# Kernel tuning notes

Measured on AMD Instinct MI355X. Metric: run time of the kernel, lower is better.

## Reference

```python
import jax, jax.numpy as jnp
import numpy as np
from jax import lax

B, C_IN, T = 256, 1, 1632
HID, CB_DIM, NUM_TOK, NUM_Q = 64, 512, 1024, 2


def conv_k2s2(x, W, b):
    # Conv1d(kernel=2, stride=2): x [B,Ci,T] -> [B,Co,T//2]; W [Co,Ci,2]
    Bx, Ci, Tx = x.shape
    xr = x.reshape(Bx, Ci, Tx // 2, 2)
    return jnp.einsum('bitk,oik->bot', xr, W) + b[None, :, None]


def convT_k2s2(x, W, b):
    # ConvTranspose1d(kernel=2, stride=2): x [B,Ci,T] -> [B,Co,2T]; W [Ci,Co,2] (torch layout)
    Bx, Ci, Tx = x.shape
    y = jnp.einsum('bit,iok->botk', x, W)  # [B,Co,T,2]
    Co = W.shape[1]
    return y.reshape(Bx, Co, 2 * Tx) + b[None, :, None]


def conv1x1(x, W, b):
    # W [Co,Ci]
    return jnp.einsum('bit,oi->bot', x, W) + b[None, :, None]


def residual_vq(x, codebooks):
    # x [B,t,D]; codebooks [NUM_Q, NUM_TOK, D]. Euclidean argmin + straight-through.
    residual = x
    quantized_out = jnp.zeros_like(x)
    all_idx, all_loss = [], []
    for q in range(codebooks.shape[0]):
        cb = codebooks[q]  # [N,D]
        # squared euclidean distance, single large GEMM
        d2 = (jnp.sum(residual ** 2, -1, keepdims=True)
              - 2.0 * jnp.einsum('btd,nd->btn', residual, cb)
              + jnp.sum(cb ** 2, -1))  # [B,t,N]
        idx = jnp.argmin(d2, axis=-1)  # [B,t]
        quant = cb[idx]  # gather [B,t,D]
        # commitment loss (codebook treated as fixed / EMA-updated)
        loss = jnp.mean((lax.stop_gradient(quant) - residual) ** 2)
        # straight-through estimator
        quant_st = residual + lax.stop_gradient(quant - residual)
        residual = residual - lax.stop_gradient(quant)
        quantized_out = quantized_out + quant_st
        all_idx.append(idx)
        all_loss.append(loss)
    return quantized_out, jnp.stack(all_idx, -1), jnp.stack(all_loss)


def setup_inputs() -> dict:
    key = jax.random.key(0)
    ks = jax.random.split(key, 16)
    s = 0.02
    return {
        'img': jax.random.normal(ks[0], (B, C_IN, T), jnp.float32),
        'W_e1': jax.random.normal(ks[1], (HID, C_IN, 2), jnp.float32) * s,
        'b_e1': jnp.zeros((HID,), jnp.float32),
        'W_e2': jax.random.normal(ks[2], (HID, HID, 2), jnp.float32) * s,
        'b_e2': jnp.zeros((HID,), jnp.float32),
        'W_e3': jax.random.normal(ks[3], (CB_DIM, HID), jnp.float32) * s,
        'b_e3': jnp.zeros((CB_DIM,), jnp.float32),
        'codebooks': jax.random.normal(ks[4], (NUM_Q, NUM_TOK, CB_DIM), jnp.float32),
        'Wt_d1': jax.random.normal(ks[5], (CB_DIM, HID, 2), jnp.float32) * s,
        'b_d1': jnp.zeros((HID,), jnp.float32),
        'Wt_d2': jax.random.normal(ks[6], (HID, HID, 2), jnp.float32) * s,
        'b_d2': jnp.zeros((HID,), jnp.float32),
        'W_d3': jax.random.normal(ks[7], (C_IN, HID), jnp.float32) * s,
        'b_d3': jnp.zeros((C_IN,), jnp.float32),
    }


def reference(img, W_e1, b_e1, W_e2, b_e2, W_e3, b_e3, codebooks,
              Wt_d1, b_d1, Wt_d2, b_d2, W_d3, b_d3):
    # encoder
    h = jax.nn.relu(conv_k2s2(img, W_e1, b_e1))
    h = jax.nn.relu(conv_k2s2(h, W_e2, b_e2))
    encoded = conv1x1(h, W_e3, b_e3)  # [B,512,408]
    # residual VQ over tokens
    x = jnp.transpose(encoded, (0, 2, 1))  # b c t -> b t c
    quantized, indices, commit_loss = residual_vq(x, codebooks)
    quantized = jnp.transpose(quantized, (0, 2, 1))  # b t c -> b c t
    # decoder
    d = jax.nn.relu(convT_k2s2(quantized, Wt_d1, b_d1))
    d = jax.nn.relu(convT_k2s2(d, Wt_d2, b_d2))
    out = conv1x1(d, W_d3, b_d3)  # [B,1,1632]
    recon_loss = jnp.mean((img - out) ** 2)
    return out, recon_loss, commit_loss, indices, quantized
```

## Files before the change

### kernel.cpp

```cpp
#include <hip/hip_runtime.h>

#define NB    256
#define TLEN  1632
#define HIDC  64
#define CBD   512
#define NTOK  1024
#define T2L   816
#define T4L   408
#define MTOK  (NB*T4L)
#define M2TOK (NB*T2L)
#define MOUT  (NB*TLEN)

#define DO_OUT    ((size_t)0)
#define DO_RECON  ((size_t)417792)
#define DO_IDX    ((size_t)417795)
#define DO_QUANT  ((size_t)626691)

typedef unsigned short u16;
typedef unsigned long long u64;
typedef __attribute__((ext_vector_type(8))) short short8;
typedef __attribute__((ext_vector_type(4))) float f32x4;
typedef __attribute__((ext_vector_type(8))) _Float16 half8;
typedef __attribute__((ext_vector_type(4))) _Float16 half4;

static constexpr size_t OFF_XR  = 0;
static constexpr size_t OFF_H1  = OFF_XR + (size_t)MTOK*512;
static constexpr size_t OFF_H2  = OFF_H1 + (size_t)NB*T2L*64;
static constexpr size_t OFF_BE2 = OFF_H2 + (size_t)NB*T4L*64;
static constexpr size_t OFF_BD1 = OFF_BE2 + 8192;
static constexpr size_t OFF_BD2 = OFF_BD1 + 65536;
static constexpr size_t OFF_BX1 = OFF_BD2 + 8192;
static constexpr size_t OFF_BX2 = OFF_BX1 + 128;
static constexpr size_t OFF_ZB  = OFF_BX2 + 128;
static constexpr size_t OFF_C2  = OFF_ZB + 128;
static constexpr size_t OFF_SLOT= OFF_C2 + 2048;
static constexpr size_t OFF_IDXI= OFF_SLOT + 1536;
static constexpr size_t OFF_KEYS= OFF_IDXI + (size_t)MTOK*2;
static constexpr size_t OFF_FC  = OFF_KEYS + (size_t)MTOK*4;
static constexpr size_t OFF_FLAG= OFF_FC + 4;
static constexpr size_t OFF_CBH = OFF_FLAG + (size_t)MTOK*2;
static constexpr size_t OFF_CBL = OFF_CBH + 524288;
static constexpr size_t OFF_P0  = OFF_CBL + 524288;
static constexpr size_t OFF_P1  = OFF_P0 + 131072;
static constexpr size_t OFF_PAIRS = OFF_P1 + 131072;

__device__ inline u64 shfl_xor_u64_w16(u64 v, int m) {
    unsigned lo = (unsigned)v, hi = (unsigned)(v >> 32);
    lo = __shfl_xor(lo, m, 16);
    hi = __shfl_xor(hi, m, 16);
    return (((u64)hi) << 32) | lo;
}
__device__ inline u64 packkey(float d, int n) {
    unsigned u = __float_as_uint(d);
    u = (u & 0x80000000u) ? ~u : (u | 0x80000000u);
    return (((u64)u) << 32) | (unsigned)n;
}
__device__ inline float unpackd(u64 k) {
    unsigned u = (unsigned)(k >> 32);
    u = (u & 0x80000000u) ? (u & 0x7fffffffu) : ~u;
    return __uint_as_float(u);
}
__device__ inline void merge2(u64& k1, u64& k2, u64 o1, u64 o2) {
    u64 n1 = (k1 < o1) ? k1 : o1;
    u64 hi = (k1 < o1) ? o1 : k1;
    u64 cand = (k1 <= o1) ? k2 : o2;
    u64 n2 = (hi < cand) ? hi : cand;
    k1 = n1; k2 = n2;
}
__device__ inline half4 cvt_h4(float4 v) {
    half4 h;
    h.x = (_Float16)v.x; h.y = (_Float16)v.y;
    h.z = (_Float16)v.z; h.w = (_Float16)v.w;
    return h;
}
__device__ inline half8 cvt_h8(float4 v0, float4 v1) {
    half8 h;
    h[0] = (_Float16)v0.x; h[1] = (_Float16)v0.y;
    h[2] = (_Float16)v0.z; h[3] = (_Float16)v0.w;
    h[4] = (_Float16)v1.x; h[5] = (_Float16)v1.y;
    h[6] = (_Float16)v1.z; h[7] = (_Float16)v1.w;
    return h;
}
__device__ inline void gll16(const u16* g, u16* l) {
    __builtin_amdgcn_global_load_lds((const __attribute__((address_space(1))) void*)g,
                                     (__attribute__((address_space(3))) void*)l, 16, 0, 0);
}

__global__ void setup_kernel(const float* __restrict__ We2, const float* __restrict__ Wtd1,
                             const float* __restrict__ Wtd2, const float* __restrict__ bd1,
                             const float* __restrict__ bd2, const float* __restrict__ cbs,
                             float* __restrict__ Be2, float* __restrict__ Bd1,
                             float* __restrict__ Bd2, float* __restrict__ bx1, float* __restrict__ bx2,
                             u16* __restrict__ cbh, float* __restrict__ c2) {
    size_t t = (size_t)blockIdx.x * 256 + threadIdx.x;
    {
        float4 v = *(const float4*)(cbs + t * 4);
        *(half4*)&cbh[t * 4] = cvt_h4(v);
    }
    {
        int w = (int)(t >> 6);
        int lane = threadIdx.x & 63;
        if (w < 2048) {
            const float* r = cbs + (size_t)w * 512;
            float4 a = *(const float4*)(r + lane * 8);
            float4 b = *(const float4*)(r + lane * 8 + 4);
            float s = a.x*a.x + a.y*a.y + a.z*a.z + a.w*a.w + b.x*b.x + b.y*b.y + b.z*b.z + b.w*b.w;
            #pragma unroll
            for (int o = 32; o > 0; o >>= 1) s += __shfl_down(s, o, 64);
            if (lane == 0) c2[w] = s;
        }
    }
    size_t stride = (size_t)gridDim.x * 256;
    for (size_t x = t; x < 64 * 128; x += stride) {
        int c = (int)(x >> 7), k = (int)(x & 127);
        Be2[x] = We2[c * 128 + ((k & 63) << 1) + (k >> 6)];
    }
    for (size_t x = t; x < 128 * 512; x += stride) {
        int n = (int)(x >> 9), k = (int)(x & 511);
        Bd1[x] = Wtd1[k * 128 + n];
    }
    for (size_t x = t; x < 128 * 64; x += stride) {
        int n = (int)(x >> 6), k = (int)(x & 63);
        Bd2[x] = Wtd2[k * 128 + n];
    }
    for (size_t x = t; x < 128; x += stride) { bx1[x] = bd1[x >> 1]; bx2[x] = bd2[x >> 1]; }
}

__global__ void enc1_kernel(const float* __restrict__ img, const float* __restrict__ W,
                            const float* __restrict__ bias, float* __restrict__ h1) {
    int idx = blockIdx.x * 256 + threadIdx.x;
    int c = idx & 63;
    int t = (idx >> 6) % T2L;
    int b = idx / (64 * T2L);
    float v = W[c * 2] * img[(size_t)b * TLEN + 2 * t] +
              W[c * 2 + 1] * img[(size_t)b * TLEN + 2 * t + 1] + bias[c];
    h1[idx] = fmaxf(v, 0.f);
}

__global__ __launch_bounds__(256) void gemm_nt(const float* __restrict__ A, const float* __restrict__ Bw,
                        const float* __restrict__ bias, float* __restrict__ C,
                        int M, int N, int K, int amode, int relu) {
    __shared__ float As[32][132];
    __shared__ float Bs[32][68];
    int m0 = blockIdx.x * 128;
    int n0 = blockIdx.y * 64;
    int tid = threadIdx.x;
    int tx = tid & 15;
    int ty = tid >> 4;
    float acc[8][4];
    #pragma unroll
    for (int i = 0; i < 8; ++i)
        #pragma unroll
        for (int j = 0; j < 4; ++j) acc[i][j] = 0.f;

    for (int k0 = 0; k0 < K; k0 += 32) {
        #pragma unroll
        for (int i = 0; i < 4; ++i) {
            int idx = tid + i * 256;
            int row = idx >> 3;
            int kq = idx & 7;
            int m = m0 + row;
            size_t base;
            if (amode == 0) base = (size_t)m * K;
            else            base = (size_t)(((m / T4L) * T2L + 2 * (m % T4L)) * 64);
            float4 v = *(const float4*)(A + base + k0 + kq * 4);
            int kk = kq * 4;
            As[kk + 0][row] = v.x; As[kk + 1][row] = v.y;
            As[kk + 2][row] = v.z; As[kk + 3][row] = v.w;
        }
        #pragma unroll
        for (int i = 0; i < 2; ++i) {
            int idx = tid + i * 256;
            int row = idx >> 3;
            int kq = idx & 7;
            float4 v = *(const float4*)(Bw + (size_t)(n0 + row) * K + k0 + kq * 4);
            int kk = kq * 4;
            Bs[kk + 0][row] = v.x; Bs[kk + 1][row] = v.y;
            Bs[kk + 2][row] = v.z; Bs[kk + 3][row] = v.w;
        }
        __syncthreads();
        #pragma unroll
        for (int kk = 0; kk < 32; ++kk) {
            float a[8], bf[4];
            float4 a0 = *(const float4*)&As[kk][ty * 8];
            float4 a1 = *(const float4*)&As[kk][ty * 8 + 4];
            a[0]=a0.x; a[1]=a0.y; a[2]=a0.z; a[3]=a0.w;
            a[4]=a1.x; a[5]=a1.y; a[6]=a1.z; a[7]=a1.w;
            float4 b0 = *(const float4*)&Bs[kk][tx * 4];
            bf[0]=b0.x; bf[1]=b0.y; bf[2]=b0.z; bf[3]=b0.w;
            #pragma unroll
            for (int i = 0; i < 8; ++i)
                #pragma unroll
                for (int j = 0; j < 4; ++j) acc[i][j] += a[i] * bf[j];
        }
        __syncthreads();
    }
    #pragma unroll
    for (int i = 0; i < 8; ++i) {
        int m = m0 + ty * 8 + i;
        float4 v;
        v.x = acc[i][0] + bias[n0 + tx * 4 + 0];
        v.y = acc[i][1] + bias[n0 + tx * 4 + 1];
        v.z = acc[i][2] + bias[n0 + tx * 4 + 2];
        v.w = acc[i][3] + bias[n0 + tx * 4 + 3];
        if (relu) { v.x=fmaxf(v.x,0.f); v.y=fmaxf(v.y,0.f); v.z=fmaxf(v.z,0.f); v.w=fmaxf(v.w,0.f); }
        *(float4*)(C + (size_t)m * N + n0 + tx * 4) = v;
    }
}

template<int Q1>
__global__ __launch_bounds__(256, 2) void vq_f16_db(
    const float* __restrict__ Ap, const u16* __restrict__ cbh,
    const float* __restrict__ c2, const u64* __restrict__ prevkeys,
    const u16* __restrict__ cb0h, u64* __restrict__ pairs)
{
    __shared__ __align__(16) u16 As[2][128 * 40];
    __shared__ __align__(16) u16 Bs[2][256 * 32];
    int tid = threadIdx.x;
    int n0 = blockIdx.x * 256, m0 = blockIdx.y * 128;
    int lane = tid & 63, wid = tid >> 6;
    int lm = lane & 15, quad = lane >> 4;
    int wm = wid >> 1, wn = wid & 1;

    f32x4 acc[4][8];
    #pragma unroll
    for (int i = 0; i < 4; ++i)
        #pragma unroll
        for (int j = 0; j < 8; ++j) acc[i][j] = (f32x4){0.f, 0.f, 0.f, 0.f};

    int ar[2], acq[2], coffA[2];
    #pragma unroll
    for (int i = 0; i < 2; ++i) {
        int idx = tid + i * 256;
        ar[i] = idx >> 2; acq[i] = idx & 3;
        coffA[i] = 0;
        if (Q1) coffA[i] = (int)(prevkeys[m0 + ar[i]] & 0xFFFFFFFFull) * 512;
    }
    int brow[4], bchk[4];
    #pragma unroll
    for (int i = 0; i < 4; ++i) {
        brow[i] = i * 64 + wid * 16 + (lane >> 2);
        bchk[i] = (lane & 3) ^ ((brow[i] >> 1) & 3);
    }

#define VQ_GLLB(BUF, K0)                                                              \
    _Pragma("unroll")                                                                 \
    for (int i = 0; i < 4; ++i) {                                                     \
        const u16* gp = cbh + (size_t)(n0 + brow[i]) * 512 + (K0) + bchk[i] * 8;      \
        gll16(gp, &Bs[BUF][i * 2048 + wid * 512]);                                    \
    }

#define VQ_LOADA(K0, V0, V1, CH)                                                      \
    _Pragma("unroll")                                                                 \
    for (int i = 0; i < 2; ++i) {                                                     \
        const float* s = Ap + (size_t)(m0 + ar[i]) * 512 + (K0) + acq[i] * 8;         \
        V0[i] = *(const float4*)s;                                                    \
        V1[i] = *(const float4*)(s + 4);                                              \
        if (Q1) CH[i] = *(const half8*)(cb0h + coffA[i] + (K0) + acq[i] * 8);         \
    }

#define VQ_WRITEA(BUF, V0, V1, CH)                                                    \
    _Pragma("unroll")                                                                 \
    for (int i = 0; i < 2; ++i) {                                                     \
        half8 hv = cvt_h8(V0[i], V1[i]);                                              \
        if (Q1) hv = hv - CH[i];                                                      \
        *(half8*)&As[BUF][ar[i] * 40 + acq[i] * 8] = hv;                              \
    }

#define VQ_COMPUTE(BUF) {                                                             \
        half8 ah[4];                                                                  \
        _Pragma("unroll")                                                             \
        for (int mt = 0; mt < 4; ++mt)                                                \
            ah[mt] = *(const half8*)&As[BUF][(wm*64 + mt*16 + lm) * 40 + quad * 8];   \
        _Pragma("unroll")                                                             \
        for (int nt = 0; nt < 8; ++nt) {                                              \
            int rn = wn * 128 + nt * 16 + lm;                                         \
            half8 bh = *(const half8*)&Bs[BUF][rn * 32 + ((quad ^ ((rn >> 1) & 3)) * 8)]; \
            _Pragma("unroll")                                                         \
            for (int mt = 0; mt < 4; ++mt)                                            \
                acc[mt][nt] = __builtin_amdgcn_mfma_f32_16x16x32_f16(ah[mt], bh, acc[mt][nt], 0, 0, 0); \
        }                                                                             \
    }

    float4 v0A[2], v1A[2], v0B[2], v1B[2];
    half8 chA[2], chB[2];
    (void)chA; (void)chB;

    VQ_GLLB(0, 0);
    VQ_LOADA(0, v0A, v1A, chA);
    VQ_WRITEA(0, v0A, v1A, chA);
    VQ_LOADA(32, v0B, v1B, chB);
    __syncthreads();

    for (int tp = 0; tp < 8; ++tp) {
        {
            VQ_GLLB(1, (2 * tp + 1) * 32);
            VQ_WRITEA(1, v0B, v1B, chB);
            if (tp < 7) { VQ_LOADA((2 * tp + 2) * 32, v0A, v1A, chA); }
            VQ_COMPUTE(0);
            __syncthreads();
        }
        {
            if (tp < 7) {
                VQ_GLLB(0, (2 * tp + 2) * 32);
                VQ_WRITEA(0, v0A, v1A, chA);
                VQ_LOADA((2 * tp + 3) * 32, v0B, v1B, chB);
            }
            VQ_COMPUTE(1);
            __syncthreads();
        }
    }
#undef VQ_GLLB
#undef VQ_LOADA
#undef VQ_WRITEA
#undef VQ_COMPUTE

    float c2v[8];
    #pragma unroll
    for (int nt = 0; nt < 8; ++nt) c2v[nt] = c2[n0 + wn * 128 + nt * 16 + lm];

    u64* scr = (u64*)&As[0][0];
    #pragma unroll
    for (int mt = 0; mt < 4; ++mt) {
        #pragma unroll
        for (int rg = 0; rg < 4; ++rg) {
            int tl = wm * 64 + mt * 16 + quad * 4 + rg;
            u64 k1 = ~0ull, k2 = ~0ull;
            #pragma unroll
            for (int nt = 0; nt < 8; ++nt) {
                float d = c2v[nt] - 2.0f * acc[mt][nt][rg];
                u64 k = packkey(d, n0 + wn * 128 + nt * 16 + lm);
                if (k < k1) { k2 = k1; k1 = k; } else if (k < k2) { k2 = k; }
            }
            #pragma unroll
            for (int s = 1; s < 16; s <<= 1) {
                u64 o1 = shfl_xor_u64_w16(k1, s);
                u64 o2 = shfl_xor_u64_w16(k2, s);
                merge2(k1, k2, o1, o2);
            }
            if (lm == 0) { scr[wn * 256 + tl * 2] = k1; scr[wn * 256 + tl * 2 + 1] = k2; }
        }
    }
    __syncthreads();
    if (tid < 128) {
        u64 a1 = scr[tid * 2], a2 = scr[tid * 2 + 1];
        merge2(a1, a2, scr[256 + tid * 2], scr[256 + tid * 2 + 1]);
        size_t base = (size_t)(m0 + tid) * 8 + blockIdx.x * 2;
        pairs[base] = a1; pairs[base + 1] = a2;
    }
}

__global__ void vq_reduce(const u64* __restrict__ pairs, u64* __restrict__ keybuf,
                          int* __restrict__ fc, int* __restrict__ flaglist, float tau) {
    int m = blockIdx.x * 256 + threadIdx.x;
    const u64* p = pairs + (size_t)m * 8;
    u64 k1 = ~0ull, k2 = ~0ull;
    #pragma unroll
    for (int i = 0; i < 8; ++i) {
        u64 k = p[i];
        if (k < k1) { k2 = k1; k1 = k; } else if (k < k2) { k2 = k; }
    }
    keybuf[m] = k1;
    if (unpackd(k2) - unpackd(k1) < tau) {
        int pos = atomicAdd(fc, 1);
        flaglist[pos] = m;
    }
}

__global__ void vq_rescue(const float* __restrict__ xr, const float* __restrict__ cb,
                          const float* __restrict__ c2, const float* __restrict__ cb0,
                          const u64* __restrict__ prevkeys,
                          const int* __restrict__ fc, const int* __restrict__ flaglist,
                          u64* __restrict__ keybuf) {
    __shared__ u64 red[4];
    int cnt = *fc;
    int lane = threadIdx.x & 63, wid = threadIdx.x >> 6;
    for (int f = blockIdx.x; f < cnt; f += gridDim.x) {
        int m = flaglist[f];
        float4 rv0 = *(const float4*)(xr + (size_t)m * 512 + lane * 8);
        float4 rv1 = *(const float4*)(xr + (size_t)m * 512 + lane * 8 + 4);
        if (cb0) {
            size_t co = (size_t)(prevkeys[m] & 0xFFFFFFFFull) * 512;
            float4 c0 = *(const float4*)(cb0 + co + lane * 8);
            float4 c1 = *(const float4*)(cb0 + co + lane * 8 + 4);
            rv0.x -= c0.x; rv0.y -= c0.y; rv0.z -= c0.z; rv0.w -= c0.w;
            rv1.x -= c1.x; rv1.y -= c1.y; rv1.z -= c1.z; rv1.w -= c1.w;
        }
        u64 best = ~0ull;
        for (int c = wid * 256; c < wid * 256 + 256; ++c) {
            const float* cp = cb + (size_t)c * 512 + lane * 8;
            float4 c0 = *(const float4*)cp;
            float4 c1 = *(const float4*)(cp + 4);
            float p = rv0.x*c0.x + rv0.y*c0.y + rv0.z*c0.z + rv0.w*c0.w
                    + rv1.x*c1.x + rv1.y*c1.y + rv1.z*c1.z + rv1.w*c1.w;
            #pragma unroll
            for (int s = 1; s < 64; s <<= 1) p += __shfl_xor(p, s, 64);
            u64 k = packkey(c2[c] - 2.0f * p, c);
            if (k < best) best = k;
        }
        if (lane == 0) red[wid] = best;
        __syncthreads();
        if (threadIdx.x == 0) {
            u64 b = red[0];
            if (red[1] < b) b = red[1];
            if (red[2] < b) b = red[2];
            if (red[3] < b) b = red[3];
            keybuf[m] = b;
        }
        __syncthreads();
    }
}

__global__ void commit_idx_kernel(const float* __restrict__ xr,
                                  const float* __restrict__ cb0f, const float* __restrict__ cb1f,
                                  const u64* __restrict__ keys0, const u64* __restrict__ keys1,
                                  float* __restrict__ idx_f, int* __restrict__ idx_i,
                                  float* __restrict__ slots) {
    int tid = threadIdx.x;
    int lane = tid & 63;
    int m = blockIdx.x * 4 + (tid >> 6);
    unsigned i0 = (unsigned)(keys0[m] & 0xFFFFFFFFull);
    unsigned i1 = (unsigned)(keys1[m] & 0xFFFFFFFFull);
    const float* x = xr + (size_t)m * 512 + lane * 8;
    const float* c0 = cb0f + (size_t)i0 * 512 + lane * 8;
    const float* c1 = cb1f + (size_t)i1 * 512 + lane * 8;
    float4 x0 = *(const float4*)x, x1 = *(const float4*)(x + 4);
    float4 a0 = *(const float4*)c0, a1 = *(const float4*)(c0 + 4);
    float4 b0 = *(const float4*)c1, b1 = *(const float4*)(c1 + 4);
    x0.x -= a0.x; x0.y -= a0.y; x0.z -= a0.z; x0.w -= a0.w;
    x1.x -= a1.x; x1.y -= a1.y; x1.z -= a1.z; x1.w -= a1.w;
    float s1 = x0.x*x0.x + x0.y*x0.y + x0.z*x0.z + x0.w*x0.w
             + x1.x*x1.x + x1.y*x1.y + x1.z*x1.z + x1.w*x1.w;
    x0.x -= b0.x; x0.y -= b0.y; x0.z -= b0.z; x0.w -= b0.w;
    x1.x -= b1.x; x1.y -= b1.y; x1.z -= b1.z; x1.w -= b1.w;
    float s2 = x0.x*x0.x + x0.y*x0.y + x0.z*x0.z + x0.w*x0.w
             + x1.x*x1.x + x1.y*x1.y + x1.z*x1.z + x1.w*x1.w;
    #pragma unroll
    for (int o = 32; o > 0; o >>= 1) { s1 += __shfl_down(s1, o, 64); s2 += __shfl_down(s2, o, 64); }
    if (lane == 0) {
        atomicAdd(&slots[512 + (m & 511)], s1);
        atomicAdd(&slots[1024 + (m & 511)], s2);
        idx_f[(size_t)m * 2]     = (float)i0;
        idx_f[(size_t)m * 2 + 1] = (float)i1;
        idx_i[m * 2] = (int)i0;
        idx_i[m * 2 + 1] = (int)i1;
    }
}

__global__ void quant_out_kernel(const float* __restrict__ cb0, const float* __restrict__ cb1,
                                 const int* __restrict__ idxi, float* __restrict__ out4) {
    __shared__ float buf[64][129];
    __shared__ int i0s[64], i1s[64];
    int b = blockIdx.x;
    int t0 = blockIdx.y * 64;
    int c0 = blockIdx.z * 128;
    int tid = threadIdx.x;
    if (tid < 64) {
        int t = t0 + tid;
        int i0 = 0, i1 = 0;
        if (t < T4L) { i0 = idxi[(b * T4L + t) * 2]; i1 = idxi[(b * T4L + t) * 2 + 1]; }
        i0s[tid] = i0; i1s[tid] = i1;
    }
    __syncthreads();
    int cl = tid & 127, th = tid >> 7;
    for (int t = th; t < 64; t += 2) {
        if (t0 + t < T4L)
            buf[t][cl] = cb0[(size_t)i0s[t] * 512 + c0 + cl] + cb1[(size_t)i1s[t] * 512 + c0 + cl];
    }
    __syncthreads();
    int lane = tid & 63, ch = tid >> 6;
    for (int cc = ch; cc < 128; cc += 4) {
        int t = t0 + lane;
        if (t < T4L) out4[((size_t)b * 512 + c0 + cc) * T4L + t] = buf[lane][cc];
    }
}

__global__ void d1_gather_kernel(const float* __restrict__ P0, const float* __restrict__ P1,
                                 const int* __restrict__ idxi, const float* __restrict__ bx1,
                                 float* __restrict__ d1) {
    int x = blockIdx.x * 256 + threadIdx.x;
    int n = x & 127;
    int m = x >> 7;
    int b = m / T4L, t = m % T4L;
    int i0 = idxi[m * 2], i1 = idxi[m * 2 + 1];
    float v = P0[i0 * 128 + n] + P1[i1 * 128 + n] + bx1[n];
    v = fmaxf(v, 0.f);
    d1[((size_t)(b * T2L + 2 * t + (n & 1))) * 64 + (n >> 1)] = v;
}

__global__ __launch_bounds__(256) void dec2_fused(
    const float* __restrict__ d1, const float* __restrict__ Bd2, const float* __restrict__ bx2,
    const float* __restrict__ W3, const float* __restrict__ b3, const float* __restrict__ img,
    float* __restrict__ out, float* __restrict__ slots)
{
    __shared__ float As[32][132];
    __shared__ float Bs[32][132];
    __shared__ float w3s[64];
    int m0 = blockIdx.x * 128;
    int tid = threadIdx.x;
    int tx = tid & 15;
    int ty = tid >> 4;
    if (tid < 64) w3s[tid] = W3[tid];
    float acc[8][8];
    #pragma unroll
    for (int i = 0; i < 8; ++i)
        #pragma unroll
        for (int j = 0; j < 8; ++j) acc[i][j] = 0.f;

    for (int k0 = 0; k0 < 64; k0 += 32) {
        #pragma unroll
        for (int i = 0; i < 4; ++i) {
            int idx = tid + i * 256;
            int row = idx >> 3;
            int kq = idx & 7;
            float4 v = *(const float4*)(d1 + (size_t)(m0 + row) * 64 + k0 + kq * 4);
            int kk = kq * 4;
            As[kk + 0][row] = v.x; As[kk + 1][row] = v.y;
            As[kk + 2][row] = v.z; As[kk + 3][row] = v.w;
        }
        #pragma unroll
        for (int i = 0; i < 4; ++i) {
            int idx = tid + i * 256;
            int row = idx >> 3;
            int kq = idx & 7;
            float4 v = *(const float4*)(Bd2 + (size_t)row * 64 + k0 + kq * 4);
            int kk = kq * 4;
            Bs[kk + 0][row] = v.x; Bs[kk + 1][row] = v.y;
            Bs[kk + 2][row] = v.z; Bs[kk + 3][row] = v.w;
        }
        __syncthreads();
        #pragma unroll
        for (int kk = 0; kk < 32; ++kk) {
            float a[8], bf[8];
            float4 a0 = *(const float4*)&As[kk][ty * 8];
            float4 a1 = *(const float4*)&As[kk][ty * 8 + 4];
            a[0]=a0.x; a[1]=a0.y; a[2]=a0.z; a[3]=a0.w;
            a[4]=a1.x; a[5]=a1.y; a[6]=a1.z; a[7]=a1.w;
            float4 b0 = *(const float4*)&Bs[kk][tx * 4];
            float4 b1 = *(const float4*)&Bs[kk][64 + tx * 4];
            bf[0]=b0.x; bf[1]=b0.y; bf[2]=b0.z; bf[3]=b0.w;
            bf[4]=b1.x; bf[5]=b1.y; bf[6]=b1.z; bf[7]=b1.w;
            #pragma unroll
            for (int i = 0; i < 8; ++i)
                #pragma unroll
                for (int j = 0; j < 8; ++j) acc[i][j] += a[i] * bf[j];
        }
        __syncthreads();
    }
    float bb3 = b3[0];
    float local = 0.f;
    #pragma unroll
    for (int i = 0; i < 8; ++i) {
        float s0 = 0.f, s1 = 0.f;
        #pragma unroll
        for (int j = 0; j < 4; ++j) {
            int n = tx * 4 + j;
            float v = fmaxf(acc[i][j] + bx2[n], 0.f);
            float w = w3s[n >> 1];
            if (j & 1) s1 += w * v; else s0 += w * v;
            int n2 = 64 + tx * 4 + j;
            float v2 = fmaxf(acc[i][j + 4] + bx2[n2], 0.f);
            float w2 = w3s[n2 >> 1];
            if (j & 1) s1 += w2 * v2; else s0 += w2 * v2;
        }
        #pragma unroll
        for (int o = 8; o > 0; o >>= 1) { s0 += __shfl_down(s0, o, 16); s1 += __shfl_down(s1, o, 16); }
        if (tx == 0) {
            int m = m0 + ty * 8 + i;
            int b = m / T2L, t2 = m % T2L;
            size_t o0 = (size_t)b * TLEN + 2 * t2;
            float v0 = s0 + bb3, v1 = s1 + bb3;
            out[o0] = v0; out[o0 + 1] = v1;
            float e0 = img[o0] - v0, e1 = img[o0 + 1] - v1;
            local += e0 * e0 + e1 * e1;
        }
    }
    if (tx == 0) atomicAdd(&slots[(blockIdx.x * 16 + ty) & 511], local);
}

__global__ void finalize_kernel(const float* __restrict__ slots, float* __restrict__ out_scalars) {
    __shared__ float red[256];
    int tid = threadIdx.x;
    for (int which = 0; which < 3; ++which) {
        float s = slots[which * 512 + tid] + slots[which * 512 + tid + 256];
        red[tid] = s; __syncthreads();
        for (int st = 128; st > 0; st >>= 1) { if (tid < st) red[tid] += red[tid + st]; __syncthreads(); }
        if (tid == 0) {
            float denom = (which == 0) ? (float)MOUT : (float)((size_t)MTOK * 512);
            out_scalars[which] = red[0] / denom;
        }
        __syncthreads();
    }
}

extern "C" void kernel_launch(void* const* d_in, const int* in_sizes, int n_in,
                              void* d_out, int out_size, void* d_ws, size_t ws_size,
                              hipStream_t stream) {
    const float* img  = (const float*)d_in[0];
    const float* We1  = (const float*)d_in[1];
    const float* be1  = (const float*)d_in[2];
    const float* We2  = (const float*)d_in[3];
    const float* be2  = (const float*)d_in[4];
    const float* We3  = (const float*)d_in[5];
    const float* be3  = (const float*)d_in[6];
    const float* cbs  = (const float*)d_in[7];
    const float* Wtd1 = (const float*)d_in[8];
    const float* bd1  = (const float*)d_in[9];
    const float* Wtd2 = (const float*)d_in[10];
    const float* bd2  = (const float*)d_in[11];
    const float* Wd3  = (const float*)d_in[12];
    const float* bd3  = (const float*)d_in[13];

    float* w = (float*)d_ws;
    float* xr   = w + OFF_XR;
    float* h1   = w + OFF_H1;
    float* h2   = w + OFF_H2;
    float* Be2  = w + OFF_BE2;
    float* Bd1  = w + OFF_BD1;
    float* Bd2  = w + OFF_BD2;
    float* bx1  = w + OFF_BX1;
    float* bx2  = w + OFF_BX2;
    float* zerob= w + OFF_ZB;
    float* c2   = w + OFF_C2;
    float* slots= w + OFF_SLOT;
    int*   idxi = (int*)(w + OFF_IDXI);
    u64*   keys = (u64*)(w + OFF_KEYS);
    int*   fc   = (int*)(w + OFF_FC);
    int*   flag = (int*)(w + OFF_FLAG);
    u16*   cbh  = (u16*)(w + OFF_CBH);
    float* P0   = w + OFF_P0;
    float* P1   = w + OFF_P1;
    u64*   pairs= (u64*)(w + OFF_PAIRS);

    float* outp = (float*)d_out;
    float* out0   = outp + DO_OUT;
    float* oscal  = outp + DO_RECON;
    float* idxf   = outp + DO_IDX;
    float* qout   = outp + DO_QUANT;

    hipMemsetAsync(slots, 0, 1536 * sizeof(float), stream);
    hipMemsetAsync(fc, 0, 2 * sizeof(int), stream);
    hipMemsetAsync(zerob, 0, 128 * sizeof(float), stream);

    setup_kernel<<<1024, 256, 0, stream>>>(We2, Wtd1, Wtd2, bd1, bd2, cbs,
                                           Be2, Bd1, Bd2, bx1, bx2, cbh, c2);

    const float* cb1p = cbs + (size_t)NTOK * CBD;

    gemm_nt<<<dim3(8, 2), 256, 0, stream>>>(cbs,  Bd1, zerob, P0, 1024, 128, 512, 0, 0);
    gemm_nt<<<dim3(8, 2), 256, 0, stream>>>(cb1p, Bd1, zerob, P1, 1024, 128, 512, 0, 0);

    enc1_kernel<<<(NB * T2L * HIDC) / 256, 256, 0, stream>>>(img, We1, be1, h1);
    gemm_nt<<<dim3(MTOK / 128, 1), 256, 0, stream>>>(h1, Be2, be2, h2, MTOK, 64, 128, 1, 1);
    gemm_nt<<<dim3(MTOK / 128, 8), 256, 0, stream>>>(h2, We3, be3, xr, MTOK, 512, 64, 0, 0);

    vq_f16_db<0><<<dim3(4, MTOK / 128), 256, 0, stream>>>(xr, cbh, c2, nullptr, nullptr, pairs);
    vq_reduce<<<MTOK / 256, 256, 0, stream>>>(pairs, keys, fc + 0, flag, 0.05f);
    vq_rescue<<<1024, 256, 0, stream>>>(xr, cbs, c2, nullptr, nullptr, fc + 0, flag, keys);
    vq_f16_db<1><<<dim3(4, MTOK / 128), 256, 0, stream>>>(xr, cbh + (size_t)NTOK * 512,
                                                          c2 + NTOK, keys, cbh, pairs);
    vq_reduce<<<MTOK / 256, 256, 0, stream>>>(pairs, keys + MTOK, fc + 1, flag + MTOK, 0.15f);
    vq_rescue<<<1024, 256, 0, stream>>>(xr, cb1p, c2 + NTOK, cbs, keys, fc + 1, flag + MTOK, keys + MTOK);

    commit_idx_kernel<<<MTOK / 4, 256, 0, stream>>>(xr, cbs, cb1p, keys, keys + MTOK, idxf, idxi, slots);

    quant_out_kernel<<<dim3(NB, 7, 4), 256, 0, stream>>>(cbs, cb1p, idxi, qout);

    d1_gather_kernel<<<(MTOK * 128) / 256, 256, 0, stream>>>(P0, P1, idxi, bx1, h1);
    dec2_fused<<<M2TOK / 128, 256, 0, stream>>>(h1, Bd2, bx2, Wd3, bd3, img, out0, slots);

    finalize_kernel<<<1, 256, 0, stream>>>(slots, oscal);
}
```

Measured before the change: 1.163 ms.

## Feed VQ GEMM with precomputed fp16 activations via direct global-to-LDS loads

The encoder's final GEMM epilogue now also writes an fp16 copy of the encoded tokens. A small r1_prep kernel computes the fp16 first-stage residual up front. Both VQ passes then stream their A operand with global_load_lds into a swizzled 32-wide LDS tile, instead of loading fp32, converting and storing through registers, which simplifies the double-buffered loop. The fp16 scratch lives in the not-yet-written idx/quant region of the output buffer. The costs are an extra kernel, extra fp16 writes, and dependence on that region being overwritten later.

```diff
diff --git a/kernel.cpp b/kernel.cpp
--- a/kernel.cpp
+++ b/kernel.cpp
@@ -15,6 +15,8 @@
 #define DO_RECON  ((size_t)417792)
 #define DO_IDX    ((size_t)417795)
 #define DO_QUANT  ((size_t)626691)
+#define DO_XRH    ((size_t)417796)
+#define DO_R1H    (DO_XRH + (size_t)MTOK*256)
 
 typedef unsigned short u16;
 typedef unsigned long long u64;
@@ -73,14 +75,6 @@
     h.z = (_Float16)v.z; h.w = (_Float16)v.w;
     return h;
 }
-__device__ inline half8 cvt_h8(float4 v0, float4 v1) {
-    half8 h;
-    h[0] = (_Float16)v0.x; h[1] = (_Float16)v0.y;
-    h[2] = (_Float16)v0.z; h[3] = (_Float16)v0.w;
-    h[4] = (_Float16)v1.x; h[5] = (_Float16)v1.y;
-    h[6] = (_Float16)v1.z; h[7] = (_Float16)v1.w;
-    return h;
-}
 __device__ inline void gll16(const u16* g, u16* l) {
     __builtin_amdgcn_global_load_lds((const __attribute__((address_space(1))) void*)g,
                                      (__attribute__((address_space(3))) void*)l, 16, 0, 0);
@@ -139,7 +133,7 @@
 
 __global__ __launch_bounds__(256) void gemm_nt(const float* __restrict__ A, const float* __restrict__ Bw,
                         const float* __restrict__ bias, float* __restrict__ C,
-                        int M, int N, int K, int amode, int relu) {
+                        int M, int N, int K, int amode, int relu, u16* __restrict__ xh) {
     __shared__ float As[32][132];
     __shared__ float Bs[32][68];
     int m0 = blockIdx.x * 128;
@@ -205,16 +199,27 @@
         v.w = acc[i][3] + bias[n0 + tx * 4 + 3];
         if (relu) { v.x=fmaxf(v.x,0.f); v.y=fmaxf(v.y,0.f); v.z=fmaxf(v.z,0.f); v.w=fmaxf(v.w,0.f); }
         *(float4*)(C + (size_t)m * N + n0 + tx * 4) = v;
-    }
-}
-
-template<int Q1>
-__global__ __launch_bounds__(256, 2) void vq_f16_db(
-    const float* __restrict__ Ap, const u16* __restrict__ cbh,
-    const float* __restrict__ c2, const u64* __restrict__ prevkeys,
-    const u16* __restrict__ cb0h, u64* __restrict__ pairs)
+        if (xh) *(half4*)&xh[(size_t)m * N + n0 + tx * 4] = cvt_h4(v);
+    }
+}
+
+__global__ void r1_prep(const u16* __restrict__ xrh, const u16* __restrict__ cbh0,
+                        const u64* __restrict__ keys, u16* __restrict__ r1h) {
+    int m = blockIdx.x * 8 + (threadIdx.x >> 5);
+    int l = threadIdx.x & 31;
+    int i0 = (int)(keys[m] & 0xFFFFFFFFull);
+    const half8* xp = (const half8*)(xrh + (size_t)m * 512 + l * 16);
+    const half8* cp = (const half8*)(cbh0 + (size_t)i0 * 512 + l * 16);
+    half8* rp = (half8*)(r1h + (size_t)m * 512 + l * 16);
+    rp[0] = xp[0] - cp[0];
+    rp[1] = xp[1] - cp[1];
+}
+
+__global__ __launch_bounds__(256, 2) void vq_f16_gll(
+    const u16* __restrict__ Ah, const u16* __restrict__ cbh,
+    const float* __restrict__ c2, u64* __restrict__ pairs)
 {
-    __shared__ __align__(16) u16 As[2][128 * 40];
+    __shared__ __align__(16) u16 As[2][128 * 32];
     __shared__ __align__(16) u16 Bs[2][256 * 32];
     int tid = threadIdx.x;
     int n0 = blockIdx.x * 256, m0 = blockIdx.y * 128;
@@ -228,13 +233,12 @@
         #pragma unroll
         for (int j = 0; j < 8; ++j) acc[i][j] = (f32x4){0.f, 0.f, 0.f, 0.f};
 
-    int ar[2], acq[2], coffA[2];
+    int arow[2], achk[2];
     #pragma unroll
     for (int i = 0; i < 2; ++i) {
-        int idx = tid + i * 256;
-        ar[i] = idx >> 2; acq[i] = idx & 3;
-        coffA[i] = 0;
-        if (Q1) coffA[i] = (int)(prevkeys[m0 + ar[i]] & 0xFFFFFFFFull) * 512;
+        int slot = wid * 128 + i * 64 + lane;
+        arow[i] = slot >> 2;
+        achk[i] = (slot & 3) ^ ((arow[i] >> 1) & 3);
     }
     int brow[4], bchk[4];
     #pragma unroll
@@ -243,35 +247,25 @@
         bchk[i] = (lane & 3) ^ ((brow[i] >> 1) & 3);
     }
 
-#define VQ_GLLB(BUF, K0)                                                              \
-    _Pragma("unroll")                                                                 \
-    for (int i = 0; i < 4; ++i) {                                                     \
-        const u16* gp = cbh + (size_t)(n0 + brow[i]) * 512 + (K0) + bchk[i] * 8;      \
-        gll16(gp, &Bs[BUF][i * 2048 + wid * 512]);                                    \
-    }
-
-#define VQ_LOADA(K0, V0, V1, CH)                                                      \
-    _Pragma("unroll")                                                                 \
-    for (int i = 0; i < 2; ++i) {                                                     \
-        const float* s = Ap + (size_t)(m0 + ar[i]) * 512 + (K0) + acq[i] * 8;         \
-        V0[i] = *(const float4*)s;                                                    \
-        V1[i] = *(const float4*)(s + 4);                                              \
-        if (Q1) CH[i] = *(const half8*)(cb0h + coffA[i] + (K0) + acq[i] * 8);         \
-    }
-
-#define VQ_WRITEA(BUF, V0, V1, CH)                                                    \
-    _Pragma("unroll")                                                                 \
-    for (int i = 0; i < 2; ++i) {                                                     \
-        half8 hv = cvt_h8(V0[i], V1[i]);                                              \
-        if (Q1) hv = hv - CH[i];                                                      \
-        *(half8*)&As[BUF][ar[i] * 40 + acq[i] * 8] = hv;                              \
+#define VQ_GLL(BUF, K0)                                                               \
+    {                                                                                 \
+        _Pragma("unroll")                                                             \
+        for (int i = 0; i < 2; ++i)                                                   \
+            gll16(Ah + (size_t)(m0 + arow[i]) * 512 + (K0) + achk[i] * 8,             \
+                  &As[BUF][wid * 1024 + i * 512]);                                    \
+        _Pragma("unroll")                                                             \
+        for (int i = 0; i < 4; ++i)                                                   \
+            gll16(cbh + (size_t)(n0 + brow[i]) * 512 + (K0) + bchk[i] * 8,            \
+                  &Bs[BUF][i * 2048 + wid * 512]);                                    \
     }
 
 #define VQ_COMPUTE(BUF) {                                                             \
         half8 ah[4];                                                                  \
         _Pragma("unroll")                                                             \
-        for (int mt = 0; mt < 4; ++mt)                                                \
-            ah[mt] = *(const half8*)&As[BUF][(wm*64 + mt*16 + lm) * 40 + quad * 8];   \
+        for (int mt = 0; mt < 4; ++mt) {                                              \
+            int r = wm * 64 + mt * 16 + lm;                                           \
+            ah[mt] = *(const half8*)&As[BUF][r * 32 + ((quad ^ ((r >> 1) & 3)) * 8)]; \
+        }                                                                             \
         _Pragma("unroll")                                                             \
         for (int nt = 0; nt < 8; ++nt) {                                              \
             int rn = wn * 128 + nt * 16 + lm;                                         \
@@ -282,37 +276,15 @@
         }                                                                             \
     }
 
-    float4 v0A[2], v1A[2], v0B[2], v1B[2];
-    half8 chA[2], chB[2];
-    (void)chA; (void)chB;
-
-    VQ_GLLB(0, 0);
-    VQ_LOADA(0, v0A, v1A, chA);
-    VQ_WRITEA(0, v0A, v1A, chA);
-    VQ_LOADA(32, v0B, v1B, chB);
+    VQ_GLL(0, 0);
     __syncthreads();
-
-    for (int tp = 0; tp < 8; ++tp) {
-        {
-            VQ_GLLB(1, (2 * tp + 1) * 32);
-            VQ_WRITEA(1, v0B, v1B, chB);
-            if (tp < 7) { VQ_LOADA((2 * tp + 2) * 32, v0A, v1A, chA); }
-            VQ_COMPUTE(0);
-            __syncthreads();
-        }
-        {
-            if (tp < 7) {
-                VQ_GLLB(0, (2 * tp + 2) * 32);
-                VQ_WRITEA(0, v0A, v1A, chA);
-                VQ_LOADA((2 * tp + 3) * 32, v0B, v1B, chB);
-            }
-            VQ_COMPUTE(1);
-            __syncthreads();
-        }
-    }
-#undef VQ_GLLB
-#undef VQ_LOADA
-#undef VQ_WRITEA
+    for (int t = 0; t < 16; ++t) {
+        int buf = t & 1;
+        if (t < 15) VQ_GLL(buf ^ 1, (t + 1) * 32);
+        VQ_COMPUTE(buf);
+        __syncthreads();
+    }
+#undef VQ_GLL
 #undef VQ_COMPUTE
 
     float c2v[8];
@@ -637,6 +609,8 @@
     float* oscal  = outp + DO_RECON;
     float* idxf   = outp + DO_IDX;
     float* qout   = outp + DO_QUANT;
+    u16*   xrh    = (u16*)(outp + DO_XRH);
+    u16*   r1h    = (u16*)(outp + DO_R1H);
 
     hipMemsetAsync(slots, 0, 1536 * sizeof(float), stream);
     hipMemsetAsync(fc, 0, 2 * sizeof(int), stream);
@@ -647,18 +621,18 @@
 
     const float* cb1p = cbs + (size_t)NTOK * CBD;
 
-    gemm_nt<<<dim3(8, 2), 256, 0, stream>>>(cbs,  Bd1, zerob, P0, 1024, 128, 512, 0, 0);
-    gemm_nt<<<dim3(8, 2), 256, 0, stream>>>(cb1p, Bd1, zerob, P1, 1024, 128, 512, 0, 0);
+    gemm_nt<<<dim3(8, 2), 256, 0, stream>>>(cbs,  Bd1, zerob, P0, 1024, 128, 512, 0, 0, nullptr);
+    gemm_nt<<<dim3(8, 2), 256, 0, stream>>>(cb1p, Bd1, zerob, P1, 1024, 128, 512, 0, 0, nullptr);
 
     enc1_kernel<<<(NB * T2L * HIDC) / 256, 256, 0, stream>>>(img, We1, be1, h1);
-    gemm_nt<<<dim3(MTOK / 128, 1), 256, 0, stream>>>(h1, Be2, be2, h2, MTOK, 64, 128, 1, 1);
-    gemm_nt<<<dim3(MTOK / 128, 8), 256, 0, stream>>>(h2, We3, be3, xr, MTOK, 512, 64, 0, 0);
-
-    vq_f16_db<0><<<dim3(4, MTOK / 128), 256, 0, stream>>>(xr, cbh, c2, nullptr, nullptr, pairs);
+    gemm_nt<<<dim3(MTOK / 128, 1), 256, 0, stream>>>(h1, Be2, be2, h2, MTOK, 64, 128, 1, 1, nullptr);
+    gemm_nt<<<dim3(MTOK / 128, 8), 256, 0, stream>>>(h2, We3, be3, xr, MTOK, 512, 64, 0, 0, xrh);
+
+    vq_f16_gll<<<dim3(4, MTOK / 128), 256, 0, stream>>>(xrh, cbh, c2, pairs);
     vq_reduce<<<MTOK / 256, 256, 0, stream>>>(pairs, keys, fc + 0, flag, 0.05f);
     vq_rescue<<<1024, 256, 0, stream>>>(xr, cbs, c2, nullptr, nullptr, fc + 0, flag, keys);
-    vq_f16_db<1><<<dim3(4, MTOK / 128), 256, 0, stream>>>(xr, cbh + (size_t)NTOK * 512,
-                                                          c2 + NTOK, keys, cbh, pairs);
+    r1_prep<<<MTOK / 8, 256, 0, stream>>>(xrh, cbh, keys, r1h);
+    vq_f16_gll<<<dim3(4, MTOK / 128), 256, 0, stream>>>(r1h, cbh + (size_t)NTOK * 512, c2 + NTOK, pairs);
     vq_reduce<<<MTOK / 256, 256, 0, stream>>>(pairs, keys + MTOK, fc + 1, flag + MTOK, 0.15f);
     vq_rescue<<<1024, 256, 0, stream>>>(xr, cb1p, c2 + NTOK, cbs, keys, fc + 1, flag + MTOK, keys + MTOK);
 
```

Result: slower. 1.239 ms (+6.5%).
